# Optimization experiments

Measured on AMD Instinct MI355X. Metric: run time of the kernel, lower is better.

The kernel has to match this reference:

```python
import jax, jax.numpy as jnp
from jax import lax
import numpy as np


def _lstm_layer(x, Wih, Whh, bih, bhh):
    """Single-direction LSTM layer, PyTorch gate order (i, f, g, o).
    x: [B, T, D_in] -> hidden sequence [B, T, H]."""
    B, T, _ = x.shape
    H = Whh.shape[1]
    # Precompute input contribution for all timesteps: [B, T, 4H]
    xw = jnp.einsum('btd,gd->btg', x, Wih) + bih + bhh

    def step(carry, xt):
        h, c = carry
        gates = xt + h @ Whh.T  # [B, 4H]
        i, f, g, o = jnp.split(gates, 4, axis=-1)
        i = jax.nn.sigmoid(i)
        f = jax.nn.sigmoid(f)
        g = jnp.tanh(g)
        o = jax.nn.sigmoid(o)
        c = f * c + i * g
        h = o * jnp.tanh(c)
        return (h, c), h

    h0 = jnp.zeros((B, H), dtype=x.dtype)
    c0 = jnp.zeros((B, H), dtype=x.dtype)
    _, hs = lax.scan(step, (h0, c0), jnp.swapaxes(xw, 0, 1))  # [T, B, H]
    return jnp.swapaxes(hs, 0, 1)  # [B, T, H]


def setup_inputs() -> dict:
    key = jax.random.key(0)
    ks = jax.random.split(key, 9)
    B, T, D, H = 64, 2048, 256, 128
    s = 1.0 / np.sqrt(H)  # PyTorch uniform(-1/sqrt(H), 1/sqrt(H)) init scale
    u = lambda k, shp: jax.random.uniform(k, shp, jnp.float32, -s, s)
    return {
        'x': jax.random.normal(ks[0], (B, T, D), jnp.float32),
        'Wih0': u(ks[1], (4 * H, D)),
        'Whh0': u(ks[2], (4 * H, H)),
        'bih0': u(ks[3], (4 * H,)),
        'bhh0': u(ks[4], (4 * H,)),
        'Wih1': u(ks[5], (4 * H, H)),
        'Whh1': u(ks[6], (4 * H, H)),
        'bih1': u(ks[7], (4 * H,)),
        'bhh1': u(ks[8], (4 * H,)),
    }


def reference(x, Wih0, Whh0, bih0, bhh0, Wih1, Whh1, bih1, bhh1):
    # 2-layer stacked LSTM; inter-layer dropout (p=0.1) is identity at eval.
    h1 = _lstm_layer(x, Wih0, Whh0, bih0, bhh0)
    h2 = _lstm_layer(h1, Wih1, Whh1, bih1, bhh1)
    return h2
```

## Files before the change

### kernel.cpp

```cpp
#include <hip/hip_runtime.h>
#include <hip/hip_bf16.h>

#define H 128
#define FOURH 512
#define BATCH 64
#define SEQ 2048
#define TC SEQ
#define NCHUNK 128
#define NGEMMB 224

typedef _Float16 half8 __attribute__((ext_vector_type(8)));
typedef float f32x4 __attribute__((ext_vector_type(4)));

__global__ void prep_kernel(const float* __restrict__ Wih0,
                            const float* __restrict__ bih0, const float* __restrict__ bhh0,
                            const float* __restrict__ bih1, const float* __restrict__ bhh1,
                            float* __restrict__ Wt0,
                            float* __restrict__ b0, float* __restrict__ b1,
                            int* __restrict__ flags) {
    int id = blockIdx.x * 256 + threadIdx.x;
    const int N0 = 256 * 512;
    if (id < N0) {
        int k = id >> 9, n = id & 511;
        Wt0[id] = Wih0[n * 256 + k];
    } else if (id < N0 + 512) {
        int i = id - N0;
        b0[i] = bih0[i] + bhh0[i];
    } else if (id < N0 + 1024) {
        int i = id - (N0 + 512);
        b1[i] = bih1[i] + bhh1[i];
    } else if (id < N0 + 1024 + 8 + NCHUNK) {
        flags[id - (N0 + 1024)] = 0;
    }
}

__device__ __forceinline__ float sigmoid_f(float x) {
    return __builtin_amdgcn_rcpf(1.f + __expf(-x));
}
__device__ __forceinline__ float tanh_f(float x) {
    return 1.f - 2.f * __builtin_amdgcn_rcpf(__expf(2.f * x) + 1.f);
}

#define LDS_BARRIER()                                                \
    do {                                                             \
        asm volatile("s_waitcnt lgkmcnt(0)" ::: "memory");           \
        __builtin_amdgcn_s_barrier();                                \
        __builtin_amdgcn_sched_barrier(0);                           \
    } while (0)

#define BM 128
#define BN 128
#define BK 32

__global__ __launch_bounds__(512, 2) void lstm_fused_kernel(
    const float* __restrict__ x,
    const float* __restrict__ Wt0,
    const float* __restrict__ b0sum,
    float* __restrict__ G,
    const float* __restrict__ Whh0,
    const float* __restrict__ Wih1,
    const float* __restrict__ Whh1,
    const float* __restrict__ b1,
    _Float16* __restrict__ h1p,
    float* __restrict__ out,
    int* __restrict__ flags)
{
    const int tid = threadIdx.x;

    int* prodF     = flags;
    int* chunkDone = flags + 8;

    __shared__ _Float16 hbuf[2][8][136];
    __shared__ float As[BK][BM + 4];
    __shared__ float Bs[BK][BN];

    if (blockIdx.x >= 16) {
        const int j   = blockIdx.x - 16;
        const int sub = j & 31;
        const int cls = j >> 5;
        const int by  = sub >> 2;
        const int bx  = sub & 3;
        const int n0  = bx * BN;
        const int tm  = tid >> 5;
        const int tn  = tid & 31;

        int ar[2], aq[2], bkk[2], bq[2];
#pragma unroll
        for (int l = 0; l < 2; ++l) {
            int fidx = tid + l * 512;
            ar[l] = fidx >> 3; aq[l] = fidx & 7;
            bkk[l] = fidx >> 5; bq[l] = fidx & 31;
        }
        float4 bv = *(const float4*)&b0sum[n0 + tn * 4];

        for (int c = cls; c < NCHUNK; c += 7) {
            const float* aptr[2];
#pragma unroll
            for (int l = 0; l < 2; ++l) {
                int rl = by * BM + ar[l];
                int b = rl >> 4;
                int t = c * 16 + (rl & 15);
                aptr[l] = x + ((size_t)b * SEQ + t) * 256 + aq[l] * 4;
            }
            float acc[2][4][4];
#pragma unroll
            for (int rh = 0; rh < 2; ++rh)
#pragma unroll
                for (int i = 0; i < 4; ++i)
#pragma unroll
                    for (int jj = 0; jj < 4; ++jj) acc[rh][i][jj] = 0.f;

            for (int k0 = 0; k0 < 256; k0 += BK) {
                __syncthreads();
#pragma unroll
                for (int l = 0; l < 2; ++l) {
                    float4 v = *(const float4*)(aptr[l] + k0);
                    As[aq[l] * 4 + 0][ar[l]] = v.x;
                    As[aq[l] * 4 + 1][ar[l]] = v.y;
                    As[aq[l] * 4 + 2][ar[l]] = v.z;
                    As[aq[l] * 4 + 3][ar[l]] = v.w;
                }
#pragma unroll
                for (int l = 0; l < 2; ++l) {
                    float4 v = *(const float4*)(Wt0 + (size_t)(k0 + bkk[l]) * FOURH + n0 + bq[l] * 4);
                    *(float4*)&Bs[bkk[l]][bq[l] * 4] = v;
                }
                __syncthreads();
#pragma unroll
                for (int kk = 0; kk < BK; ++kk) {
                    float a[8], bb[4];
                    *(float4*)&a[0] = *(const float4*)&As[kk][tm * 4];
                    *(float4*)&a[4] = *(const float4*)&As[kk][64 + tm * 4];
                    *(float4*)&bb[0] = *(const float4*)&Bs[kk][tn * 4];
#pragma unroll
                    for (int rh = 0; rh < 2; ++rh)
#pragma unroll
                        for (int i = 0; i < 4; ++i)
#pragma unroll
                            for (int jj = 0; jj < 4; ++jj)
                                acc[rh][i][jj] = fmaf(a[rh * 4 + i], bb[jj], acc[rh][i][jj]);
                }
            }
#pragma unroll
            for (int rh = 0; rh < 2; ++rh)
#pragma unroll
                for (int i = 0; i < 4; ++i) {
                    int rl = by * BM + rh * 64 + tm * 4 + i;
                    int b = rl >> 4;
                    int t = c * 16 + (rl & 15);
                    float* gp = G + ((size_t)b * SEQ + t) * FOURH + n0 + tn * 4;
                    float4 o = make_float4(acc[rh][i][0] + bv.x, acc[rh][i][1] + bv.y,
                                           acc[rh][i][2] + bv.z, acc[rh][i][3] + bv.w);
                    *(float4*)gp = o;
                }
            __syncthreads();
            if (tid == 0) {
                __threadfence();
                __hip_atomic_fetch_add(&chunkDone[c], 1, __ATOMIC_RELEASE,
                                       __HIP_MEMORY_SCOPE_AGENT);
            }
        }
        return;
    }

    const int w  = tid >> 6;
    const int l  = tid & 63;
    const int li = l & 15;
    const int q  = l >> 4;
    const int u  = 16 * w + li;
    const int b0 = q * 2;
    const int ab = ((li >> 2) * 2) + (li & 1);

#define WAIT_FLAG(ptr, tgtv)                                                   \
    do {                                                                       \
        if (tid == 0) {                                                        \
            while (__hip_atomic_load((ptr), __ATOMIC_RELAXED,                  \
                                     __HIP_MEMORY_SCOPE_AGENT) < (tgtv))       \
                __builtin_amdgcn_s_sleep(4);                                   \
            (void)__hip_atomic_load((ptr), __ATOMIC_ACQUIRE,                   \
                                    __HIP_MEMORY_SCOPE_AGENT);                 \
        }                                                                      \
        __syncthreads();                                                       \
    } while (0)

    if (blockIdx.x < 8) {
        const int g = blockIdx.x;

        half8 Bf[4][4];
#pragma unroll
        for (int tl = 0; tl < 4; ++tl)
#pragma unroll
            for (int kf = 0; kf < 4; ++kf) {
                const float* wp = Whh0 + (size_t)(tl * 128 + u) * H + kf * 32 + q * 8;
                float4 v0 = *(const float4*)wp;
                float4 v1 = *(const float4*)(wp + 4);
                half8 b;
                b[0] = (_Float16)v0.x; b[1] = (_Float16)v0.y;
                b[2] = (_Float16)v0.z; b[3] = (_Float16)v0.w;
                b[4] = (_Float16)v1.x; b[5] = (_Float16)v1.y;
                b[6] = (_Float16)v1.z; b[7] = (_Float16)v1.w;
                Bf[tl][kf] = b;
            }

        float c0 = 0.f, c1 = 0.f, h0 = 0.f, h1v = 0.f;
        hbuf[0][b0][u]     = (_Float16)0.f;
        hbuf[0][b0 + 1][u] = (_Float16)0.f;

        const float* gb = G + (size_t)(8 * g) * TC * FOURH;
        const int voff0 = b0 * TC * FOURH + u;
        const int voff1 = (b0 + 1) * TC * FOURH + u;

        WAIT_FLAG(&chunkDone[0], 32);

        float G0[8], G1[8], G2[8], G3[8];
        const float* gld = gb;
#pragma unroll
        for (int tl = 0; tl < 4; ++tl) {
            G0[tl * 2 + 0] = gld[voff0 + tl * H];
            G0[tl * 2 + 1] = gld[voff1 + tl * H];
        }
        gld += FOURH;
#pragma unroll
        for (int tl = 0; tl < 4; ++tl) {
            G1[tl * 2 + 0] = gld[voff0 + tl * H];
            G1[tl * 2 + 1] = gld[voff1 + tl * H];
        }
        gld += FOURH;
#pragma unroll
        for (int tl = 0; tl < 4; ++tl) {
            G2[tl * 2 + 0] = gld[voff0 + tl * H];
            G2[tl * 2 + 1] = gld[voff1 + tl * H];
        }
        gld += FOURH;
#pragma unroll
        for (int tl = 0; tl < 4; ++tl) {
            G3[tl * 2 + 0] = gld[voff0 + tl * H];
            G3[tl * 2 + 1] = gld[voff1 + tl * H];
        }
        gld += FOURH;

        _Float16* php = h1p + (size_t)(8 * g + b0) * H + u;

#define P_STEP(PB, GR)                                                            \
    {                                                                             \
        half8 Afr[4];                                                             \
        _Pragma("unroll")                                                         \
        for (int kf = 0; kf < 4; ++kf)                                            \
            Afr[kf] = *(const half8*)&hbuf[PB][ab][kf * 32 + q * 8];              \
        f32x4 acc[4];                                                             \
        _Pragma("unroll")                                                         \
        for (int tl = 0; tl < 4; ++tl) {                                          \
            acc[tl][0] = GR[tl * 2 + 0]; acc[tl][1] = GR[tl * 2 + 1];             \
            acc[tl][2] = 0.f;            acc[tl][3] = 0.f;                        \
        }                                                                         \
        _Pragma("unroll")                                                         \
        for (int tl = 0; tl < 4; ++tl) {                                          \
            GR[tl * 2 + 0] = gld[voff0 + tl * H];                                 \
            GR[tl * 2 + 1] = gld[voff1 + tl * H];                                 \
        }                                                                         \
        gld += FOURH;                                                             \
        _Pragma("unroll")                                                         \
        for (int kf = 0; kf < 4; ++kf)                                            \
            _Pragma("unroll")                                                     \
            for (int tl = 0; tl < 4; ++tl)                                        \
                acc[tl] = __builtin_amdgcn_mfma_f32_16x16x32_f16(Afr[kf], Bf[tl][kf], acc[tl], 0, 0, 0); \
        {                                                                         \
            float ig = sigmoid_f(acc[0][0]);                                      \
            float fg = sigmoid_f(acc[1][0]);                                      \
            float gg = tanh_f(acc[2][0]);                                         \
            float og = sigmoid_f(acc[3][0]);                                      \
            c0 = fmaf(fg, c0, ig * gg);                                           \
            h0 = og * tanh_f(c0);                                                 \
            float ig1 = sigmoid_f(acc[0][1]);                                     \
            float fg1 = sigmoid_f(acc[1][1]);                                     \
            float gg1 = tanh_f(acc[2][1]);                                        \
            float og1 = sigmoid_f(acc[3][1]);                                     \
            c1 = fmaf(fg1, c1, ig1 * gg1);                                        \
            h1v = og1 * tanh_f(c1);                                               \
        }                                                                         \
        hbuf[PB ^ 1][b0][u]     = (_Float16)h0;                                   \
        hbuf[PB ^ 1][b0 + 1][u] = (_Float16)h1v;                                  \
        php[0]   = (_Float16)h0;                                                  \
        php[128] = (_Float16)h1v;                                                 \
        php += BATCH * H;                                                         \
        LDS_BARRIER();                                                            \
    }

        for (int s4 = 0; s4 < TC; s4 += 4) {
            if ((s4 & 15) == 0) {
                int k = (s4 >> 4) + 1;
                if (k > NCHUNK - 1) k = NCHUNK - 1;
                WAIT_FLAG(&chunkDone[k], 32);
            }
            P_STEP(0, G0)
            P_STEP(1, G1)
            P_STEP(0, G2)
            P_STEP(1, G3)
            if ((s4 & 31) == 28) {
                __threadfence();
                __syncthreads();
                if (tid == 0)
                    __hip_atomic_store(&prodF[g], s4 + 4, __ATOMIC_RELEASE,
                                       __HIP_MEMORY_SCOPE_AGENT);
            }
        }
#undef P_STEP
    } else {
        const int g = blockIdx.x - 8;

        half8 Bf[4][8];
#pragma unroll
        for (int tl = 0; tl < 4; ++tl)
#pragma unroll
            for (int kf = 0; kf < 8; ++kf) {
                const float* base = (kf < 4) ? Wih1 : Whh1;
                int kk = (kf & 3) * 32 + q * 8;
                const float* wp = base + (size_t)(tl * 128 + u) * H + kk;
                float4 v0 = *(const float4*)wp;
                float4 v1 = *(const float4*)(wp + 4);
                half8 b;
                b[0] = (_Float16)v0.x; b[1] = (_Float16)v0.y;
                b[2] = (_Float16)v0.z; b[3] = (_Float16)v0.w;
                b[4] = (_Float16)v1.x; b[5] = (_Float16)v1.y;
                b[6] = (_Float16)v1.z; b[7] = (_Float16)v1.w;
                Bf[tl][kf] = b;
            }

        float bv[4];
#pragma unroll
        for (int tl = 0; tl < 4; ++tl) bv[tl] = b1[tl * 128 + u];

        float c0 = 0.f, c1 = 0.f, h0, h1v;
        hbuf[0][b0][u]     = (_Float16)0.f;
        hbuf[0][b0 + 1][u] = (_Float16)0.f;

        const _Float16* h1pG = h1p + (size_t)(8 * g + ab) * H + q * 8;
        float* op0 = out + (size_t)(8 * g + b0) * SEQ * H + u;
        float* op1 = out + (size_t)(8 * g + b0 + 1) * SEQ * H + u;

        WAIT_FLAG(&prodF[g], 64);

        half8 Af0[4], Af1[4];
#pragma unroll
        for (int kf = 0; kf < 4; ++kf)
            Af0[kf] = *(const half8*)(h1pG + kf * 32);
        {
            const _Float16* hp = h1pG + (size_t)(BATCH * H);
#pragma unroll
            for (int kf = 0; kf < 4; ++kf)
                Af1[kf] = *(const half8*)(hp + kf * 32);
        }

#define C_STEP(S, PB, AfU)                                                        \
    {                                                                             \
        half8 Ah[4];                                                              \
        _Pragma("unroll")                                                         \
        for (int kf = 0; kf < 4; ++kf)                                            \
            Ah[kf] = *(const half8*)&hbuf[PB][ab][kf * 32 + q * 8];               \
        f32x4 acc[4];                                                             \
        _Pragma("unroll")                                                         \
        for (int tl = 0; tl < 4; ++tl) {                                          \
            acc[tl][0] = bv[tl]; acc[tl][1] = bv[tl];                             \
            acc[tl][2] = bv[tl]; acc[tl][3] = bv[tl];                             \
        }                                                                         \
        _Pragma("unroll")                                                         \
        for (int kf = 0; kf < 4; ++kf)                                            \
            _Pragma("unroll")                                                     \
            for (int tl = 0; tl < 4; ++tl)                                        \
                acc[tl] = __builtin_amdgcn_mfma_f32_16x16x32_f16(AfU[kf], Bf[tl][kf], acc[tl], 0, 0, 0); \
        {                                                                         \
            int sn = (S) + 2; if (sn > TC - 1) sn = TC - 1;                       \
            const _Float16* hp = h1pG + (size_t)sn * (BATCH * H);                 \
            _Pragma("unroll")                                                     \
            for (int kf = 0; kf < 4; ++kf)                                        \
                AfU[kf] = *(const half8*)(hp + kf * 32);                          \
        }                                                                         \
        _Pragma("unroll")                                                         \
        for (int kf = 0; kf < 4; ++kf)                                            \
            _Pragma("unroll")                                                     \
            for (int tl = 0; tl < 4; ++tl)                                        \
                acc[tl] = __builtin_amdgcn_mfma_f32_16x16x32_f16(Ah[kf], Bf[tl][kf + 4], acc[tl], 0, 0, 0); \
        {                                                                         \
            float ig = sigmoid_f(acc[0][0]);                                      \
            float fg = sigmoid_f(acc[1][0]);                                      \
            float gg = tanh_f(acc[2][0]);                                         \
            float og = sigmoid_f(acc[3][0]);                                      \
            c0 = fmaf(fg, c0, ig * gg);                                           \
            h0 = og * tanh_f(c0);                                                 \
            float ig1 = sigmoid_f(acc[0][1]);                                     \
            float fg1 = sigmoid_f(acc[1][1]);                                     \
            float gg1 = tanh_f(acc[2][1]);                                        \
            float og1 = sigmoid_f(acc[3][1]);                                     \
            c1 = fmaf(fg1, c1, ig1 * gg1);                                        \
            h1v = og1 * tanh_f(c1);                                               \
        }                                                                         \
        hbuf[PB ^ 1][b0][u]     = (_Float16)h0;                                   \
        hbuf[PB ^ 1][b0 + 1][u] = (_Float16)h1v;                                  \
        op0[0] = h0;                                                              \
        op1[0] = h1v;                                                             \
        op0 += H; op1 += H;                                                       \
        LDS_BARRIER();                                                            \
    }

        for (int s4 = 0; s4 < TC; s4 += 4) {
            if (s4 && (s4 & 31) == 0) {
                int tgt = s4 + 64; if (tgt > TC) tgt = TC;
                WAIT_FLAG(&prodF[g], tgt);
            }
            C_STEP(s4 + 0, 0, Af0)
            C_STEP(s4 + 1, 1, Af1)
            C_STEP(s4 + 2, 0, Af0)
            C_STEP(s4 + 3, 1, Af1)
        }
#undef C_STEP
    }
#undef WAIT_FLAG
}

extern "C" void kernel_launch(void* const* d_in, const int* in_sizes, int n_in,
                              void* d_out, int out_size, void* d_ws, size_t ws_size,
                              hipStream_t stream) {
    const float* x    = (const float*)d_in[0];
    const float* Wih0 = (const float*)d_in[1];
    const float* Whh0 = (const float*)d_in[2];
    const float* bih0 = (const float*)d_in[3];
    const float* bhh0 = (const float*)d_in[4];
    const float* Wih1 = (const float*)d_in[5];
    const float* Whh1 = (const float*)d_in[6];
    const float* bih1 = (const float*)d_in[7];
    const float* bhh1 = (const float*)d_in[8];
    float* out = (float*)d_out;

    char* ws = (char*)d_ws;
    size_t off = 0;
    auto carve = [&](size_t bytes) -> char* {
        char* p = ws + off;
        off += (bytes + 255) & ~(size_t)255;
        return p;
    };

    float*     Wt0   = (float*)carve(256 * 512 * 4);
    float*     b0v   = (float*)carve(512 * 4);
    float*     b1v   = (float*)carve(512 * 4);
    _Float16*  h1p   = (_Float16*)carve((size_t)SEQ * BATCH * H * 2);
    int*       flags = (int*)carve((8 + NCHUNK) * 4);
    float*     gbuf  = (float*)carve((size_t)BATCH * SEQ * FOURH * 4 + 16384);

    prep_kernel<<<517, 256, 0, stream>>>(Wih0, bih0, bhh0, bih1, bhh1, Wt0, b0v, b1v, flags);

    lstm_fused_kernel<<<240, 512, 0, stream>>>(x, Wt0, b0v, gbuf,
                                               Whh0, Wih1, Whh1, b1v,
                                               h1p, out, flags);
}
```

Measured before the change: 2.071 ms.

## Move layer-1 input projection to GEMM blocks and use ring buffers for gates

Replaces the full [B,T,4H] layer-0 gate buffer with a 256-slot ring buffer, so producers now wait on consumer progress flags. Layer-1's input projection (h1 @ Wih1) moves out of the layer-1 recurrent blocks into the GEMM worker blocks, computed in fp16 MFMA chunks into a second ring buffer. The layer-1 scan then only does the recurrent matmul per step. This shortens the serial critical path and reduces memory footprint, at the cost of more cross-block flag synchronization and the risk of producer/consumer stalls.

```diff
diff --git a/kernel.cpp b/kernel.cpp
--- a/kernel.cpp
+++ b/kernel.cpp
@@ -7,7 +7,9 @@
 #define SEQ 2048
 #define TC SEQ
 #define NCHUNK 128
-#define NGEMMB 224
+#define RSLOT 256
+#define GSTRIDE (BATCH * FOURH)
+#define D1 4
 
 typedef _Float16 half8 __attribute__((ext_vector_type(8)));
 typedef float f32x4 __attribute__((ext_vector_type(4)));
@@ -15,8 +17,10 @@
 __global__ void prep_kernel(const float* __restrict__ Wih0,
                             const float* __restrict__ bih0, const float* __restrict__ bhh0,
                             const float* __restrict__ bih1, const float* __restrict__ bhh1,
+                            const float* __restrict__ Wih1,
                             float* __restrict__ Wt0,
                             float* __restrict__ b0, float* __restrict__ b1,
+                            _Float16* __restrict__ wt1h,
                             int* __restrict__ flags) {
     int id = blockIdx.x * 256 + threadIdx.x;
     const int N0 = 256 * 512;
@@ -29,8 +33,11 @@
     } else if (id < N0 + 1024) {
         int i = id - (N0 + 512);
         b1[i] = bih1[i] + bhh1[i];
-    } else if (id < N0 + 1024 + 8 + NCHUNK) {
-        flags[id - (N0 + 1024)] = 0;
+    } else if (id < N0 + 1024 + 65536) {
+        int i = id - (N0 + 1024);
+        wt1h[i] = (_Float16)Wih1[i];
+    } else if (id < N0 + 1024 + 65536 + 272) {
+        flags[id - (N0 + 1024 + 65536)] = 0;
     }
 }
 
@@ -56,19 +63,22 @@
     const float* __restrict__ x,
     const float* __restrict__ Wt0,
     const float* __restrict__ b0sum,
-    float* __restrict__ G,
+    float* __restrict__ gring,
     const float* __restrict__ Whh0,
-    const float* __restrict__ Wih1,
+    const _Float16* __restrict__ wt1h,
     const float* __restrict__ Whh1,
     const float* __restrict__ b1,
     _Float16* __restrict__ h1p,
+    float* __restrict__ g1r,
     float* __restrict__ out,
     int* __restrict__ flags)
 {
     const int tid = threadIdx.x;
 
     int* prodF     = flags;
-    int* chunkDone = flags + 8;
+    int* consF     = flags + 8;
+    int* chunkDone = flags + 16;
+    int* g1Done    = flags + 144;
 
     __shared__ _Float16 hbuf[2][8][136];
     __shared__ float As[BK][BM + 4];
@@ -83,81 +93,151 @@
         const int n0  = bx * BN;
         const int tm  = tid >> 5;
         const int tn  = tid & 31;
+        const int wv  = tid >> 6;
+        const int l   = tid & 63;
+        const int li  = l & 15;
+        const int q   = l >> 4;
+        const int gb1 = 8 * by + wv;
 
         int ar[2], aq[2], bkk[2], bq[2];
 #pragma unroll
-        for (int l = 0; l < 2; ++l) {
-            int fidx = tid + l * 512;
-            ar[l] = fidx >> 3; aq[l] = fidx & 7;
-            bkk[l] = fidx >> 5; bq[l] = fidx & 31;
-        }
-        float4 bv = *(const float4*)&b0sum[n0 + tn * 4];
-
-        for (int c = cls; c < NCHUNK; c += 7) {
-            const float* aptr[2];
-#pragma unroll
-            for (int l = 0; l < 2; ++l) {
-                int rl = by * BM + ar[l];
-                int b = rl >> 4;
-                int t = c * 16 + (rl & 15);
-                aptr[l] = x + ((size_t)b * SEQ + t) * 256 + aq[l] * 4;
-            }
-            float acc[2][4][4];
-#pragma unroll
-            for (int rh = 0; rh < 2; ++rh)
-#pragma unroll
-                for (int i = 0; i < 4; ++i)
-#pragma unroll
-                    for (int jj = 0; jj < 4; ++jj) acc[rh][i][jj] = 0.f;
-
-            for (int k0 = 0; k0 < 256; k0 += BK) {
+        for (int l2 = 0; l2 < 2; ++l2) {
+            int fidx = tid + l2 * 512;
+            ar[l2] = fidx >> 3; aq[l2] = fidx & 7;
+            bkk[l2] = fidx >> 5; bq[l2] = fidx & 31;
+        }
+        float4 bvg = *(const float4*)&b0sum[n0 + tn * 4];
+        float bv1g[8];
+#pragma unroll
+        for (int ct = 0; ct < 8; ++ct) bv1g[ct] = b1[n0 + ct * 16 + li];
+
+        for (int idx = cls; idx < NCHUNK + D1; idx += 7) {
+            if (idx < NCHUNK) {
+                if (idx >= 16) {
+                    if (tid == 0) {
+                        while (__hip_atomic_load(&prodF[by], __ATOMIC_RELAXED,
+                                                 __HIP_MEMORY_SCOPE_AGENT) < 16 * (idx - 15))
+                            __builtin_amdgcn_s_sleep(4);
+                    }
+                    __syncthreads();
+                }
+                const float* aptr[2];
+#pragma unroll
+                for (int l2 = 0; l2 < 2; ++l2) {
+                    int rl = by * BM + ar[l2];
+                    int b = rl >> 4;
+                    int t = idx * 16 + (rl & 15);
+                    aptr[l2] = x + ((size_t)b * SEQ + t) * 256 + aq[l2] * 4;
+                }
+                float acc[2][4][4];
+#pragma unroll
+                for (int rh = 0; rh < 2; ++rh)
+#pragma unroll
+                    for (int i = 0; i < 4; ++i)
+#pragma unroll
+                        for (int jj = 0; jj < 4; ++jj) acc[rh][i][jj] = 0.f;
+
+                for (int k0 = 0; k0 < 256; k0 += BK) {
+                    __syncthreads();
+#pragma unroll
+                    for (int l2 = 0; l2 < 2; ++l2) {
+                        float4 v = *(const float4*)(aptr[l2] + k0);
+                        As[aq[l2] * 4 + 0][ar[l2]] = v.x;
+                        As[aq[l2] * 4 + 1][ar[l2]] = v.y;
+                        As[aq[l2] * 4 + 2][ar[l2]] = v.z;
+                        As[aq[l2] * 4 + 3][ar[l2]] = v.w;
+                    }
+#pragma unroll
+                    for (int l2 = 0; l2 < 2; ++l2) {
+                        float4 v = *(const float4*)(Wt0 + (size_t)(k0 + bkk[l2]) * FOURH + n0 + bq[l2] * 4);
+                        *(float4*)&Bs[bkk[l2]][bq[l2] * 4] = v;
+                    }
+                    __syncthreads();
+#pragma unroll
+                    for (int kk = 0; kk < BK; ++kk) {
+                        float a[8], bb[4];
+                        *(float4*)&a[0] = *(const float4*)&As[kk][tm * 4];
+                        *(float4*)&a[4] = *(const float4*)&As[kk][64 + tm * 4];
+                        *(float4*)&bb[0] = *(const float4*)&Bs[kk][tn * 4];
+#pragma unroll
+                        for (int rh = 0; rh < 2; ++rh)
+#pragma unroll
+                            for (int i = 0; i < 4; ++i)
+#pragma unroll
+                                for (int jj = 0; jj < 4; ++jj)
+                                    acc[rh][i][jj] = fmaf(a[rh * 4 + i], bb[jj], acc[rh][i][jj]);
+                    }
+                }
+#pragma unroll
+                for (int rh = 0; rh < 2; ++rh)
+#pragma unroll
+                    for (int i = 0; i < 4; ++i) {
+                        int rl = by * BM + rh * 64 + tm * 4 + i;
+                        int b = rl >> 4;
+                        int slot = (idx & 15) * 16 + (rl & 15);
+                        float* gp = gring + ((size_t)slot * BATCH + b) * FOURH + n0 + tn * 4;
+                        float4 o = make_float4(acc[rh][i][0] + bvg.x, acc[rh][i][1] + bvg.y,
+                                               acc[rh][i][2] + bvg.z, acc[rh][i][3] + bvg.w);
+                        *(float4*)gp = o;
+                    }
                 __syncthreads();
-#pragma unroll
-                for (int l = 0; l < 2; ++l) {
-                    float4 v = *(const float4*)(aptr[l] + k0);
-                    As[aq[l] * 4 + 0][ar[l]] = v.x;
-                    As[aq[l] * 4 + 1][ar[l]] = v.y;
-                    As[aq[l] * 4 + 2][ar[l]] = v.z;
-                    As[aq[l] * 4 + 3][ar[l]] = v.w;
-                }
-#pragma unroll
-                for (int l = 0; l < 2; ++l) {
-                    float4 v = *(const float4*)(Wt0 + (size_t)(k0 + bkk[l]) * FOURH + n0 + bq[l] * 4);
-                    *(float4*)&Bs[bkk[l]][bq[l] * 4] = v;
+                if (tid == 0) {
+                    __threadfence();
+                    __hip_atomic_fetch_add(&chunkDone[idx], 1, __ATOMIC_RELEASE,
+                                           __HIP_MEMORY_SCOPE_AGENT);
+                }
+            }
+
+            int m = idx - D1;
+            if (m >= 0 && m < NCHUNK) {
+                if (tid == 0) {
+                    while (__hip_atomic_load(&prodF[by], __ATOMIC_RELAXED,
+                                             __HIP_MEMORY_SCOPE_AGENT) < 16 * (m + 1))
+                        __builtin_amdgcn_s_sleep(4);
+                    if (m >= 16) {
+                        while (__hip_atomic_load(&consF[by], __ATOMIC_RELAXED,
+                                                 __HIP_MEMORY_SCOPE_AGENT) < 16 * (m - 15))
+                            __builtin_amdgcn_s_sleep(4);
+                    }
+                    (void)__hip_atomic_load(&prodF[by], __ATOMIC_ACQUIRE,
+                                            __HIP_MEMORY_SCOPE_AGENT);
                 }
                 __syncthreads();
-#pragma unroll
-                for (int kk = 0; kk < BK; ++kk) {
-                    float a[8], bb[4];
-                    *(float4*)&a[0] = *(const float4*)&As[kk][tm * 4];
-                    *(float4*)&a[4] = *(const float4*)&As[kk][64 + tm * 4];
-                    *(float4*)&bb[0] = *(const float4*)&Bs[kk][tn * 4];
-#pragma unroll
-                    for (int rh = 0; rh < 2; ++rh)
-#pragma unroll
-                        for (int i = 0; i < 4; ++i)
-#pragma unroll
-                            for (int jj = 0; jj < 4; ++jj)
-                                acc[rh][i][jj] = fmaf(a[rh * 4 + i], bb[jj], acc[rh][i][jj]);
-                }
-            }
-#pragma unroll
-            for (int rh = 0; rh < 2; ++rh)
-#pragma unroll
-                for (int i = 0; i < 4; ++i) {
-                    int rl = by * BM + rh * 64 + tm * 4 + i;
-                    int b = rl >> 4;
-                    int t = c * 16 + (rl & 15);
-                    float* gp = G + ((size_t)b * SEQ + t) * FOURH + n0 + tn * 4;
-                    float4 o = make_float4(acc[rh][i][0] + bv.x, acc[rh][i][1] + bv.y,
-                                           acc[rh][i][2] + bv.z, acc[rh][i][3] + bv.w);
-                    *(float4*)gp = o;
-                }
-            __syncthreads();
-            if (tid == 0) {
-                __threadfence();
-                __hip_atomic_fetch_add(&chunkDone[c], 1, __ATOMIC_RELEASE,
-                                       __HIP_MEMORY_SCOPE_AGENT);
+
+                const int t0 = m * 16;
+                half8 Af[4];
+                const _Float16* ap = h1p + ((size_t)(t0 + li) * BATCH + gb1) * H + q * 8;
+#pragma unroll
+                for (int kf = 0; kf < 4; ++kf)
+                    Af[kf] = *(const half8*)(ap + kf * 32);
+
+                f32x4 acc1[8];
+#pragma unroll
+                for (int ct = 0; ct < 8; ++ct) {
+                    acc1[ct][0] = bv1g[ct]; acc1[ct][1] = bv1g[ct];
+                    acc1[ct][2] = bv1g[ct]; acc1[ct][3] = bv1g[ct];
+                }
+#pragma unroll
+                for (int ct = 0; ct < 8; ++ct) {
+                    const _Float16* wp = wt1h + (size_t)(n0 + ct * 16 + li) * H + q * 8;
+#pragma unroll
+                    for (int kf = 0; kf < 4; ++kf) {
+                        half8 Bfr = *(const half8*)(wp + kf * 32);
+                        acc1[ct] = __builtin_amdgcn_mfma_f32_16x16x32_f16(Af[kf], Bfr, acc1[ct], 0, 0, 0);
+                    }
+                }
+                const int srow = (t0 & 255) + q * 4;
+#pragma unroll
+                for (int ct = 0; ct < 8; ++ct)
+#pragma unroll
+                    for (int i = 0; i < 4; ++i)
+                        g1r[((size_t)(srow + i) * BATCH + gb1) * FOURH + n0 + ct * 16 + li] = acc1[ct][i];
+                __syncthreads();
+                if (tid == 0) {
+                    __threadfence();
+                    __hip_atomic_fetch_add(&g1Done[m], 1, __ATOMIC_RELEASE,
+                                           __HIP_MEMORY_SCOPE_AGENT);
+                }
             }
         }
         return;
@@ -183,65 +263,7 @@
         __syncthreads();                                                       \
     } while (0)
 
-    if (blockIdx.x < 8) {
-        const int g = blockIdx.x;
-
-        half8 Bf[4][4];
-#pragma unroll
-        for (int tl = 0; tl < 4; ++tl)
-#pragma unroll
-            for (int kf = 0; kf < 4; ++kf) {
-                const float* wp = Whh0 + (size_t)(tl * 128 + u) * H + kf * 32 + q * 8;
-                float4 v0 = *(const float4*)wp;
-                float4 v1 = *(const float4*)(wp + 4);
-                half8 b;
-                b[0] = (_Float16)v0.x; b[1] = (_Float16)v0.y;
-                b[2] = (_Float16)v0.z; b[3] = (_Float16)v0.w;
-                b[4] = (_Float16)v1.x; b[5] = (_Float16)v1.y;
-                b[6] = (_Float16)v1.z; b[7] = (_Float16)v1.w;
-                Bf[tl][kf] = b;
-            }
-
-        float c0 = 0.f, c1 = 0.f, h0 = 0.f, h1v = 0.f;
-        hbuf[0][b0][u]     = (_Float16)0.f;
-        hbuf[0][b0 + 1][u] = (_Float16)0.f;
-
-        const float* gb = G + (size_t)(8 * g) * TC * FOURH;
-        const int voff0 = b0 * TC * FOURH + u;
-        const int voff1 = (b0 + 1) * TC * FOURH + u;
-
-        WAIT_FLAG(&chunkDone[0], 32);
-
-        float G0[8], G1[8], G2[8], G3[8];
-        const float* gld = gb;
-#pragma unroll
-        for (int tl = 0; tl < 4; ++tl) {
-            G0[tl * 2 + 0] = gld[voff0 + tl * H];
-            G0[tl * 2 + 1] = gld[voff1 + tl * H];
-        }
-        gld += FOURH;
-#pragma unroll
-        for (int tl = 0; tl < 4; ++tl) {
-            G1[tl * 2 + 0] = gld[voff0 + tl * H];
-            G1[tl * 2 + 1] = gld[voff1 + tl * H];
-        }
-        gld += FOURH;
-#pragma unroll
-        for (int tl = 0; tl < 4; ++tl) {
-            G2[tl * 2 + 0] = gld[voff0 + tl * H];
-            G2[tl * 2 + 1] = gld[voff1 + tl * H];
-        }
-        gld += FOURH;
-#pragma unroll
-        for (int tl = 0; tl < 4; ++tl) {
-            G3[tl * 2 + 0] = gld[voff0 + tl * H];
-            G3[tl * 2 + 1] = gld[voff1 + tl * H];
-        }
-        gld += FOURH;
-
-        _Float16* php = h1p + (size_t)(8 * g + b0) * H + u;
-
-#define P_STEP(PB, GR)                                                            \
+#define SCAN_STEP(S, PB, GR, GBASE, BOFF0, BOFF1, BFARR, STORE_STMT)              \
     {                                                                             \
         half8 Afr[4];                                                             \
         _Pragma("unroll")                                                         \
@@ -253,17 +275,19 @@
             acc[tl][0] = GR[tl * 2 + 0]; acc[tl][1] = GR[tl * 2 + 1];             \
             acc[tl][2] = 0.f;            acc[tl][3] = 0.f;                        \
         }                                                                         \
-        _Pragma("unroll")                                                         \
-        for (int tl = 0; tl < 4; ++tl) {                                          \
-            GR[tl * 2 + 0] = gld[voff0 + tl * H];                                 \
-            GR[tl * 2 + 1] = gld[voff1 + tl * H];                                 \
+        {                                                                         \
+            const float* gp_ = (GBASE) + (size_t)(((S) + 4) & (RSLOT - 1)) * GSTRIDE; \
+            _Pragma("unroll")                                                     \
+            for (int tl = 0; tl < 4; ++tl) {                                      \
+                GR[tl * 2 + 0] = gp_[(BOFF0) + tl * H];                           \
+                GR[tl * 2 + 1] = gp_[(BOFF1) + tl * H];                           \
+            }                                                                     \
         }                                                                         \
-        gld += FOURH;                                                             \
         _Pragma("unroll")                                                         \
         for (int kf = 0; kf < 4; ++kf)                                            \
             _Pragma("unroll")                                                     \
             for (int tl = 0; tl < 4; ++tl)                                        \
-                acc[tl] = __builtin_amdgcn_mfma_f32_16x16x32_f16(Afr[kf], Bf[tl][kf], acc[tl], 0, 0, 0); \
+                acc[tl] = __builtin_amdgcn_mfma_f32_16x16x32_f16(Afr[kf], BFARR[tl][kf], acc[tl], 0, 0, 0); \
         {                                                                         \
             float ig = sigmoid_f(acc[0][0]);                                      \
             float fg = sigmoid_f(acc[1][0]);                                      \
@@ -280,42 +304,19 @@
         }                                                                         \
         hbuf[PB ^ 1][b0][u]     = (_Float16)h0;                                   \
         hbuf[PB ^ 1][b0 + 1][u] = (_Float16)h1v;                                  \
-        php[0]   = (_Float16)h0;                                                  \
-        php[128] = (_Float16)h1v;                                                 \
-        php += BATCH * H;                                                         \
+        STORE_STMT                                                                \
         LDS_BARRIER();                                                            \
     }
 
-        for (int s4 = 0; s4 < TC; s4 += 4) {
-            if ((s4 & 15) == 0) {
-                int k = (s4 >> 4) + 1;
-                if (k > NCHUNK - 1) k = NCHUNK - 1;
-                WAIT_FLAG(&chunkDone[k], 32);
-            }
-            P_STEP(0, G0)
-            P_STEP(1, G1)
-            P_STEP(0, G2)
-            P_STEP(1, G3)
-            if ((s4 & 31) == 28) {
-                __threadfence();
-                __syncthreads();
-                if (tid == 0)
-                    __hip_atomic_store(&prodF[g], s4 + 4, __ATOMIC_RELEASE,
-                                       __HIP_MEMORY_SCOPE_AGENT);
-            }
-        }
-#undef P_STEP
-    } else {
-        const int g = blockIdx.x - 8;
-
-        half8 Bf[4][8];
+    if (blockIdx.x < 8) {
+        const int g = blockIdx.x;
+
+        half8 Bf[4][4];
 #pragma unroll
         for (int tl = 0; tl < 4; ++tl)
 #pragma unroll
-            for (int kf = 0; kf < 8; ++kf) {
-                const float* base = (kf < 4) ? Wih1 : Whh1;
-                int kk = (kf & 3) * 32 + q * 8;
-                const float* wp = base + (size_t)(tl * 128 + u) * H + kk;
+            for (int kf = 0; kf < 4; ++kf) {
+                const float* wp = Whh0 + (size_t)(tl * 128 + u) * H + kf * 32 + q * 8;
                 float4 v0 = *(const float4*)wp;
                 float4 v1 = *(const float4*)(wp + 4);
                 half8 b;
@@ -326,95 +327,116 @@
                 Bf[tl][kf] = b;
             }
 
-        float bv[4];
-#pragma unroll
-        for (int tl = 0; tl < 4; ++tl) bv[tl] = b1[tl * 128 + u];
+        float c0 = 0.f, c1 = 0.f, h0 = 0.f, h1v = 0.f;
+        hbuf[0][b0][u]     = (_Float16)0.f;
+        hbuf[0][b0 + 1][u] = (_Float16)0.f;
+
+        const int boff0 = (8 * g + b0) * FOURH + u;
+        const int boff1 = boff0 + FOURH;
+
+        WAIT_FLAG(&chunkDone[0], 32);
+
+        float Ga[8], Gb[8], Gc[8], Gd[8];
+#pragma unroll
+        for (int tl = 0; tl < 4; ++tl) {
+            Ga[tl * 2 + 0] = gring[(size_t)0 * GSTRIDE + boff0 + tl * H];
+            Ga[tl * 2 + 1] = gring[(size_t)0 * GSTRIDE + boff1 + tl * H];
+            Gb[tl * 2 + 0] = gring[(size_t)1 * GSTRIDE + boff0 + tl * H];
+            Gb[tl * 2 + 1] = gring[(size_t)1 * GSTRIDE + boff1 + tl * H];
+            Gc[tl * 2 + 0] = gring[(size_t)2 * GSTRIDE + boff0 + tl * H];
+            Gc[tl * 2 + 1] = gring[(size_t)2 * GSTRIDE + boff1 + tl * H];
+            Gd[tl * 2 + 0] = gring[(size_t)3 * GSTRIDE + boff0 + tl * H];
+            Gd[tl * 2 + 1] = gring[(size_t)3 * GSTRIDE + boff1 + tl * H];
+        }
+
+        _Float16* php = h1p + (size_t)(8 * g + b0) * H + u;
+
+#define P_STORE { php[0] = (_Float16)h0; php[128] = (_Float16)h1v; php += BATCH * H; }
+
+        for (int s4 = 0; s4 < TC; s4 += 4) {
+            if ((s4 & 15) == 0) {
+                int k = (s4 >> 4) + 1;
+                if (k > NCHUNK - 1) k = NCHUNK - 1;
+                WAIT_FLAG(&chunkDone[k], 32);
+            }
+            SCAN_STEP(s4 + 0, 0, Ga, gring, boff0, boff1, Bf, P_STORE)
+            SCAN_STEP(s4 + 1, 1, Gb, gring, boff0, boff1, Bf, P_STORE)
+            SCAN_STEP(s4 + 2, 0, Gc, gring, boff0, boff1, Bf, P_STORE)
+            SCAN_STEP(s4 + 3, 1, Gd, gring, boff0, boff1, Bf, P_STORE)
+            if ((s4 & 31) == 28) {
+                __threadfence();
+                __syncthreads();
+                if (tid == 0)
+                    __hip_atomic_store(&prodF[g], s4 + 4, __ATOMIC_RELEASE,
+                                       __HIP_MEMORY_SCOPE_AGENT);
+            }
+        }
+#undef P_STORE
+    } else {
+        const int g = blockIdx.x - 8;
+
+        half8 Bf[4][4];
+#pragma unroll
+        for (int tl = 0; tl < 4; ++tl)
+#pragma unroll
+            for (int kf = 0; kf < 4; ++kf) {
+                const float* wp = Whh1 + (size_t)(tl * 128 + u) * H + kf * 32 + q * 8;
+                float4 v0 = *(const float4*)wp;
+                float4 v1 = *(const float4*)(wp + 4);
+                half8 b;
+                b[0] = (_Float16)v0.x; b[1] = (_Float16)v0.y;
+                b[2] = (_Float16)v0.z; b[3] = (_Float16)v0.w;
+                b[4] = (_Float16)v1.x; b[5] = (_Float16)v1.y;
+                b[6] = (_Float16)v1.z; b[7] = (_Float16)v1.w;
+                Bf[tl][kf] = b;
+            }
 
         float c0 = 0.f, c1 = 0.f, h0, h1v;
         hbuf[0][b0][u]     = (_Float16)0.f;
         hbuf[0][b0 + 1][u] = (_Float16)0.f;
 
-        const _Float16* h1pG = h1p + (size_t)(8 * g + ab) * H + q * 8;
+        const int boff0 = (8 * g + b0) * FOURH + u;
+        const int boff1 = boff0 + FOURH;
         float* op0 = out + (size_t)(8 * g + b0) * SEQ * H + u;
         float* op1 = out + (size_t)(8 * g + b0 + 1) * SEQ * H + u;
 
-        WAIT_FLAG(&prodF[g], 64);
-
-        half8 Af0[4], Af1[4];
-#pragma unroll
-        for (int kf = 0; kf < 4; ++kf)
-            Af0[kf] = *(const half8*)(h1pG + kf * 32);
-        {
-            const _Float16* hp = h1pG + (size_t)(BATCH * H);
-#pragma unroll
-            for (int kf = 0; kf < 4; ++kf)
-                Af1[kf] = *(const half8*)(hp + kf * 32);
-        }
-
-#define C_STEP(S, PB, AfU)                                                        \
-    {                                                                             \
-        half8 Ah[4];                                                              \
-        _Pragma("unroll")                                                         \
-        for (int kf = 0; kf < 4; ++kf)                                            \
-            Ah[kf] = *(const half8*)&hbuf[PB][ab][kf * 32 + q * 8];               \
-        f32x4 acc[4];                                                             \
-        _Pragma("unroll")                                                         \
-        for (int tl = 0; tl < 4; ++tl) {                                          \
-            acc[tl][0] = bv[tl]; acc[tl][1] = bv[tl];                             \
-            acc[tl][2] = bv[tl]; acc[tl][3] = bv[tl];                             \
-        }                                                                         \
-        _Pragma("unroll")                                                         \
-        for (int kf = 0; kf < 4; ++kf)                                            \
-            _Pragma("unroll")                                                     \
-            for (int tl = 0; tl < 4; ++tl)                                        \
-                acc[tl] = __builtin_amdgcn_mfma_f32_16x16x32_f16(AfU[kf], Bf[tl][kf], acc[tl], 0, 0, 0); \
-        {                                                                         \
-            int sn = (S) + 2; if (sn > TC - 1) sn = TC - 1;                       \
-            const _Float16* hp = h1pG + (size_t)sn * (BATCH * H);                 \
-            _Pragma("unroll")                                                     \
-            for (int kf = 0; kf < 4; ++kf)                                        \
-                AfU[kf] = *(const half8*)(hp + kf * 32);                          \
-        }                                                                         \
-        _Pragma("unroll")                                                         \
-        for (int kf = 0; kf < 4; ++kf)                                            \
-            _Pragma("unroll")                                                     \
-            for (int tl = 0; tl < 4; ++tl)                                        \
-                acc[tl] = __builtin_amdgcn_mfma_f32_16x16x32_f16(Ah[kf], Bf[tl][kf + 4], acc[tl], 0, 0, 0); \
-        {                                                                         \
-            float ig = sigmoid_f(acc[0][0]);                                      \
-            float fg = sigmoid_f(acc[1][0]);                                      \
-            float gg = tanh_f(acc[2][0]);                                         \
-            float og = sigmoid_f(acc[3][0]);                                      \
-            c0 = fmaf(fg, c0, ig * gg);                                           \
-            h0 = og * tanh_f(c0);                                                 \
-            float ig1 = sigmoid_f(acc[0][1]);                                     \
-            float fg1 = sigmoid_f(acc[1][1]);                                     \
-            float gg1 = tanh_f(acc[2][1]);                                        \
-            float og1 = sigmoid_f(acc[3][1]);                                     \
-            c1 = fmaf(fg1, c1, ig1 * gg1);                                        \
-            h1v = og1 * tanh_f(c1);                                               \
-        }                                                                         \
-        hbuf[PB ^ 1][b0][u]     = (_Float16)h0;                                   \
-        hbuf[PB ^ 1][b0 + 1][u] = (_Float16)h1v;                                  \
-        op0[0] = h0;                                                              \
-        op1[0] = h1v;                                                             \
-        op0 += H; op1 += H;                                                       \
-        LDS_BARRIER();                                                            \
-    }
+        WAIT_FLAG(&g1Done[0], 32);
+
+        float Ga[8], Gb[8], Gc[8], Gd[8];
+#pragma unroll
+        for (int tl = 0; tl < 4; ++tl) {
+            Ga[tl * 2 + 0] = g1r[(size_t)0 * GSTRIDE + boff0 + tl * H];
+            Ga[tl * 2 + 1] = g1r[(size_t)0 * GSTRIDE + boff1 + tl * H];
+            Gb[tl * 2 + 0] = g1r[(size_t)1 * GSTRIDE + boff0 + tl * H];
+            Gb[tl * 2 + 1] = g1r[(size_t)1 * GSTRIDE + boff1 + tl * H];
+            Gc[tl * 2 + 0] = g1r[(size_t)2 * GSTRIDE + boff0 + tl * H];
+            Gc[tl * 2 + 1] = g1r[(size_t)2 * GSTRIDE + boff1 + tl * H];
+            Gd[tl * 2 + 0] = g1r[(size_t)3 * GSTRIDE + boff0 + tl * H];
+            Gd[tl * 2 + 1] = g1r[(size_t)3 * GSTRIDE + boff1 + tl * H];
+        }
+
+#define C_STORE { op0[0] = h0; op1[0] = h1v; op0 += H; op1 += H; }
 
         for (int s4 = 0; s4 < TC; s4 += 4) {
-            if (s4 && (s4 & 31) == 0) {
-                int tgt = s4 + 64; if (tgt > TC) tgt = TC;
-                WAIT_FLAG(&prodF[g], tgt);
-            }
-            C_STEP(s4 + 0, 0, Af0)
-            C_STEP(s4 + 1, 1, Af1)
-            C_STEP(s4 + 2, 0, Af0)
-            C_STEP(s4 + 3, 1, Af1)
-        }
-#undef C_STEP
+            if ((s4 & 15) == 0) {
+                int k = (s4 >> 4) + 1;
+                if (k > NCHUNK - 1) k = NCHUNK - 1;
+                WAIT_FLAG(&g1Done[k], 32);
+            }
+            SCAN_STEP(s4 + 0, 0, Ga, g1r, boff0, boff1, Bf, C_STORE)
+            SCAN_STEP(s4 + 1, 1, Gb, g1r, boff0, boff1, Bf, C_STORE)
+            SCAN_STEP(s4 + 2, 0, Gc, g1r, boff0, boff1, Bf, C_STORE)
+            SCAN_STEP(s4 + 3, 1, Gd, g1r, boff0, boff1, Bf, C_STORE)
+            if ((s4 & 31) == 28) {
+                if (tid == 0)
+                    __hip_atomic_store(&consF[g], s4 + 4, __ATOMIC_RELEASE,
+                                       __HIP_MEMORY_SCOPE_AGENT);
+            }
+        }
+#undef C_STORE
     }
 #undef WAIT_FLAG
+#undef SCAN_STEP
 }
 
 extern "C" void kernel_launch(void* const* d_in, const int* in_sizes, int n_in,
@@ -442,13 +464,16 @@
     float*     Wt0   = (float*)carve(256 * 512 * 4);
     float*     b0v   = (float*)carve(512 * 4);
     float*     b1v   = (float*)carve(512 * 4);
+    _Float16*  wt1h  = (_Float16*)carve(65536 * 2);
     _Float16*  h1p   = (_Float16*)carve((size_t)SEQ * BATCH * H * 2);
-    int*       flags = (int*)carve((8 + NCHUNK) * 4);
-    float*     gbuf  = (float*)carve((size_t)BATCH * SEQ * FOURH * 4 + 16384);
-
-    prep_kernel<<<517, 256, 0, stream>>>(Wih0, bih0, bhh0, bih1, bhh1, Wt0, b0v, b1v, flags);
-
-    lstm_fused_kernel<<<240, 512, 0, stream>>>(x, Wt0, b0v, gbuf,
-                                               Whh0, Wih1, Whh1, b1v,
-                                               h1p, out, flags);
+    int*       flags = (int*)carve(272 * 4);
+    float*     gring = (float*)carve((size_t)RSLOT * GSTRIDE * 4);
+    float*     g1r   = (float*)carve((size_t)RSLOT * GSTRIDE * 4);
+
+    prep_kernel<<<774, 256, 0, stream>>>(Wih0, bih0, bhh0, bih1, bhh1, Wih1,
+                                         Wt0, b0v, b1v, wt1h, flags);
+
+    lstm_fused_kernel<<<240, 512, 0, stream>>>(x, Wt0, b0v, gring,
+                                               Whh0, wt1h, Whh1, b1v,
+                                               h1p, g1r, out, flags);
 }
```

Measured after the change: 2.148 ms. 3.7% more time.
